# Kernel optimization log

Hardware: AMD Instinct MI355X
Metric: run time of the kernel (lower is better)

Reference implementation:

```python
import jax, jax.numpy as jnp
import numpy as np

D_MODEL = 512
NHEAD = 8
D_K = D_MODEL // NHEAD


def setup_inputs() -> dict:
    key = jax.random.key(0)
    ks = jax.random.split(key, 9)
    s = 1.0 / np.sqrt(D_MODEL)
    x = jax.random.normal(ks[0], (2, 2048, D_MODEL), dtype=jnp.float32)
    # torch Linear weights: [out_features, in_features]
    Wq = jax.random.uniform(ks[1], (D_MODEL, D_MODEL), jnp.float32, -s, s)
    bq = jax.random.uniform(ks[2], (D_MODEL,), jnp.float32, -s, s)
    Wk = jax.random.uniform(ks[3], (D_MODEL, D_MODEL), jnp.float32, -s, s)
    bk = jax.random.uniform(ks[4], (D_MODEL,), jnp.float32, -s, s)
    Wv = jax.random.uniform(ks[5], (D_MODEL, D_MODEL), jnp.float32, -s, s)
    bv = jax.random.uniform(ks[6], (D_MODEL,), jnp.float32, -s, s)
    Wo = jax.random.uniform(ks[7], (D_MODEL, D_MODEL), jnp.float32, -s, s)
    bo = jax.random.uniform(ks[8], (D_MODEL,), jnp.float32, -s, s)
    return {"x": x, "Wq": Wq, "bq": bq, "Wk": Wk, "bk": bk,
            "Wv": Wv, "bv": bv, "Wo": Wo, "bo": bo}


def reference(x, Wq, bq, Wk, bk, Wv, bv, Wo, bo):
    B, S, D = x.shape
    H, Dk = NHEAD, D_K

    def proj(W, b):
        # torch Linear: x @ W.T + b -> [B, S, D] -> [B, H, S, Dk]
        y = jnp.einsum('bsd,ed->bse', x, W) + b
        return y.reshape(B, S, H, Dk).transpose(0, 2, 1, 3)

    q = proj(Wq, bq)
    k = proj(Wk, bk)
    v = proj(Wv, bv)

    scores = jnp.einsum('bhqd,bhkd->bhqk', q, k) / jnp.sqrt(jnp.float32(Dk))
    attn = jax.nn.softmax(scores, axis=-1)  # explicit O(S^2) attention matrix
    out = jnp.einsum('bhqk,bhkd->bhqd', attn, v)
    out = out.transpose(0, 2, 1, 3).reshape(B, S, D)
    return jnp.einsum('bsd,ed->bse', out, Wo) + bo
```

## Files before the change

kernel.cpp:

```cpp
#include <hip/hip_runtime.h>

typedef __bf16 bf16_t;
typedef bf16_t bf16x8 __attribute__((ext_vector_type(8)));
typedef bf16_t bf16x4 __attribute__((ext_vector_type(4)));
typedef float  floatx4 __attribute__((ext_vector_type(4)));
typedef short  s16x4   __attribute__((ext_vector_type(4)));

#define D_MODEL 512
#define NHEAD   8
#define DK      64
#define BATCH   2
#define SEQ     2048
#define MTOT    (BATCH*SEQ)
#define QSCALE  0.18033688011112042591f

static __device__ __forceinline__ floatx4 mfma16(bf16x8 a, bf16x8 b, floatx4 c) {
    return __builtin_amdgcn_mfma_f32_16x16x32_bf16(a, b, c, 0, 0, 0);
}
static __device__ __forceinline__ floatx4 mfma16k16(s16x4 a, s16x4 b, floatx4 c) {
    return __builtin_amdgcn_mfma_f32_16x16x16bf16_1k(a, b, c, 0, 0, 0);
}

static __device__ __forceinline__ void glds16(bf16_t* lds, const bf16_t* g) {
    __builtin_amdgcn_global_load_lds(
        (const __attribute__((address_space(1))) unsigned int*)g,
        (__attribute__((address_space(3))) unsigned int*)lds,
        16, 0, 0);
}

__global__ __launch_bounds__(256)
void to_bf16(const float* __restrict__ x,
             const float* __restrict__ Wq, const float* __restrict__ Wk,
             const float* __restrict__ Wv, const float* __restrict__ Wo,
             bf16_t* __restrict__ xb, bf16_t* __restrict__ wqb,
             bf16_t* __restrict__ wkb, bf16_t* __restrict__ wvb,
             bf16_t* __restrict__ wob)
{
    const int blk = blockIdx.x;
    const float* src; bf16_t* dst; size_t base;
    if      (blk < 1024) { src = x;  dst = xb;  base = (size_t)blk * 2048; }
    else if (blk < 1152) { src = Wq; dst = wqb; base = (size_t)(blk - 1024) * 2048; }
    else if (blk < 1280) { src = Wk; dst = wkb; base = (size_t)(blk - 1152) * 2048; }
    else if (blk < 1408) { src = Wv; dst = wvb; base = (size_t)(blk - 1280) * 2048; }
    else                 { src = Wo; dst = wob; base = (size_t)(blk - 1408) * 2048; }
    const size_t off = base + (size_t)threadIdx.x * 8;
    const float4 a = *(const float4*)(src + off);
    const float4 b = *(const float4*)(src + off + 4);
    bf16x8 p;
    p[0]=(bf16_t)a.x; p[1]=(bf16_t)a.y; p[2]=(bf16_t)a.z; p[3]=(bf16_t)a.w;
    p[4]=(bf16_t)b.x; p[5]=(bf16_t)b.y; p[6]=(bf16_t)b.z; p[7]=(bf16_t)b.w;
    const size_t off2 = off ^ ((((off >> 10) & 3)) << 3);
    *(bf16x8*)(dst + off2) = p;
}

__global__ __launch_bounds__(256)
void qkv_proj(const bf16_t* __restrict__ xb,
              const bf16_t* __restrict__ wqb, const float* __restrict__ bq,
              const bf16_t* __restrict__ wkb, const float* __restrict__ bk,
              const bf16_t* __restrict__ wvb, const float* __restrict__ bv,
              bf16_t* __restrict__ q_ws, bf16_t* __restrict__ k_ws,
              bf16_t* __restrict__ vt_ws)
{
    __shared__ bf16_t As[64 * 32];
    __shared__ bf16_t Bs[128 * 32];

    const int mtile = blockIdx.x;
    const int ntile = blockIdx.y;
    const int which = ntile >> 2;
    const int nsub  = ntile & 3;
    const bf16_t* W   = (which == 0) ? wqb : (which == 1) ? wkb : wvb;
    const float* bias = (which == 0) ? bq  : (which == 1) ? bk  : bv;

    const int tid  = threadIdx.x;
    const int lane = tid & 63;
    const int wave = tid >> 6;
    const int wm = wave & 1, wn = wave >> 1;
    const int l15 = lane & 15, quad = lane >> 4;
    const int m0 = mtile * 64;
    const int n0 = nsub * 128;
    const int lr = lane >> 2;
    const int lc = (lane & 3) * 8;
    const int csw = (quad ^ ((l15 >> 1) & 3)) * 8;

    floatx4 acc[2][4] = {};

    for (int k0 = 0; k0 < 512; k0 += 32) {
        __syncthreads();
        glds16(&As[wave * 16 * 32], xb + (size_t)(m0 + wave * 16 + lr) * 512 + k0 + lc);
        #pragma unroll
        for (int q = 0; q < 2; ++q) {
            const int r = wave * 32 + q * 16;
            glds16(&Bs[r * 32], W + (size_t)(n0 + r + lr) * 512 + k0 + lc);
        }
        __syncthreads();

        bf16x8 af[2], bfr[4];
        #pragma unroll
        for (int i = 0; i < 2; ++i)
            af[i] = *(const bf16x8*)(&As[(wm * 32 + i * 16 + l15) * 32 + csw]);
        #pragma unroll
        for (int j = 0; j < 4; ++j)
            bfr[j] = *(const bf16x8*)(&Bs[(wn * 64 + j * 16 + l15) * 32 + csw]);
        #pragma unroll
        for (int i = 0; i < 2; ++i)
            #pragma unroll
            for (int j = 0; j < 4; ++j)
                acc[i][j] = mfma16(af[i], bfr[j], acc[i][j]);
    }

    #pragma unroll
    for (int j = 0; j < 4; ++j) {
        const int e = n0 + wn * 64 + j * 16 + l15;
        const float be = bias[e];
        const int h = e >> 6, d = e & 63;
        #pragma unroll
        for (int i = 0; i < 2; ++i) {
            const int mbase = m0 + wm * 32 + i * 16 + quad * 4;
            const int b = mbase >> 11;
            const int sl = mbase & 2047;
            floatx4 c = acc[i][j];
            if (which == 2) {
                bf16x4 pk;
                #pragma unroll
                for (int r = 0; r < 4; ++r) pk[r] = (bf16_t)(c[r] + be);
                const int slz = (sl & ~63) | ((((sl >> 3) & 7) ^ (d & 7)) << 3) | (sl & 7);
                *(bf16x4*)(vt_ws + ((size_t)((b * 8 + h) * 64 + d)) * 2048 + slz) = pk;
            } else if (which == 1) {
                #pragma unroll
                for (int r = 0; r < 4; ++r) {
                    const int s = sl + r;
                    const int dz = ((((d >> 3) ^ (s & 7))) << 3) | (d & 7);
                    k_ws[(size_t)(b * 8 + h) * (SEQ * DK) + (size_t)s * 64 + dz] =
                        (bf16_t)(c[r] + be);
                }
            } else {
                #pragma unroll
                for (int r = 0; r < 4; ++r)
                    q_ws[(size_t)(b * 8 + h) * (SEQ * DK) + (size_t)(sl + r) * 64 + d] =
                        (bf16_t)((c[r] + be) * QSCALE);
            }
        }
    }
}

__global__ __launch_bounds__(512, 4)
void attn_kernel(const bf16_t* __restrict__ q_ws, const bf16_t* __restrict__ k_ws,
                 const bf16_t* __restrict__ vt_ws, bf16_t* __restrict__ attn_ws)
{
    __shared__ bf16_t Kt[4][64 * 64];
    __shared__ bf16_t Vt[4][64 * 64];

    const int bh = blockIdx.x;
    const int qt = blockIdx.y;
    const int tid = threadIdx.x, lane = tid & 63, wave = tid >> 6;
    const int l15 = lane & 15, quad = lane >> 4;
    const int g  = wave & 3;
    const int wq = wave >> 2;

    const bf16_t* Qb  = q_ws  + (size_t)bh * SEQ * DK;
    const bf16_t* Kb  = k_ws  + (size_t)bh * SEQ * DK;
    const bf16_t* Vtb = vt_ws + (size_t)bh * DK * SEQ;

    const int sp = wave & 3;
    bf16_t* stile = (wave < 4) ? &Kt[sp][0] : &Vt[sp][0];
    const int srow8 = lane >> 3;
    const int scol  = (lane & 7) * 8;

    bf16x8 aq[2][2];
    #pragma unroll
    for (int mt = 0; mt < 2; ++mt)
        #pragma unroll
        for (int c = 0; c < 2; ++c)
            aq[mt][c] = *(const bf16x8*)(Qb +
                (size_t)(qt * 64 + wq * 32 + mt * 16 + l15) * 64 + c * 32 + quad * 8);

    floatx4 O[2][4] = {};
    float rs[2] = {0.f, 0.f};
    const int ksw0 = ((0 + quad) ^ (l15 & 7)) * 8;
    const int ksw1 = ((4 + quad) ^ (l15 & 7)) * 8;

    for (int t = 0; t < 8; ++t) {
        __syncthreads();
        {
            const int kg = t * 256 + sp * 64;
            if (wave < 4) {
                #pragma unroll
                for (int i = 0; i < 8; ++i)
                    glds16(stile + i * 512,
                           Kb + (size_t)(kg + i * 8 + srow8) * 64 + scol);
            } else {
                #pragma unroll
                for (int i = 0; i < 8; ++i)
                    glds16(stile + i * 512,
                           Vtb + (size_t)(i * 8 + srow8) * 2048 + kg + scol);
            }
        }
        __syncthreads();

        s16x4 pf[2][4];
        #pragma unroll
        for (int kf = 0; kf < 4; ++kf) {
            const bf16_t* krow = &Kt[g][(kf * 16 + l15) * 64];
            bf16x8 k0 = *(const bf16x8*)(krow + ksw0);
            bf16x8 k1 = *(const bf16x8*)(krow + ksw1);
            #pragma unroll
            for (int mt = 0; mt < 2; ++mt) {
                floatx4 z = {0.f, 0.f, 0.f, 0.f};
                z = mfma16(k0, aq[mt][0], z);
                z = mfma16(k1, aq[mt][1], z);
                bf16x4 pk;
                float s = 0.f;
                #pragma unroll
                for (int r = 0; r < 4; ++r) {
                    const float p = __builtin_amdgcn_exp2f(z[r]);
                    s += p;
                    pk[r] = (bf16_t)p;
                }
                rs[mt] += s;
                pf[mt][kf] = __builtin_bit_cast(s16x4, pk);
            }
        }

        #pragma unroll
        for (int kg2 = 0; kg2 < 4; ++kg2) {
            const int voff = (((kg2 * 2 + (quad >> 1)) ^ (l15 & 7)) * 8) + (quad & 1) * 4;
            #pragma unroll
            for (int df = 0; df < 4; ++df) {
                const s16x4 v = *(const s16x4*)(&Vt[g][(df * 16 + l15) * 64 + voff]);
                #pragma unroll
                for (int mt = 0; mt < 2; ++mt)
                    O[mt][df] = mfma16k16(pf[mt][kg2], v, O[mt][df]);
            }
        }
    }

    #pragma unroll
    for (int mt = 0; mt < 2; ++mt) {
        rs[mt] += __shfl_xor(rs[mt], 16, 64);
        rs[mt] += __shfl_xor(rs[mt], 32, 64);
    }

    float* scratch = (float*)&Kt[0][0];
    __syncthreads();
    if (g >= 2) {
        float* s = scratch + (size_t)((wq * 2 + (g - 2)) * 64 + lane) * 35;
        #pragma unroll
        for (int mt = 0; mt < 2; ++mt) {
            #pragma unroll
            for (int df = 0; df < 4; ++df)
                #pragma unroll
                for (int r = 0; r < 4; ++r) s[mt * 16 + df * 4 + r] = O[mt][df][r];
            s[32 + mt] = rs[mt];
        }
    }
    __syncthreads();
    if (g < 2) {
        const float* s = scratch + (size_t)((wq * 2 + g) * 64 + lane) * 35;
        #pragma unroll
        for (int mt = 0; mt < 2; ++mt) {
            #pragma unroll
            for (int df = 0; df < 4; ++df)
                #pragma unroll
                for (int r = 0; r < 4; ++r) O[mt][df][r] += s[mt * 16 + df * 4 + r];
            rs[mt] += s[32 + mt];
        }
    }
    __syncthreads();
    if (g == 1) {
        float* s = scratch + (size_t)(wq * 64 + lane) * 35;
        #pragma unroll
        for (int mt = 0; mt < 2; ++mt) {
            #pragma unroll
            for (int df = 0; df < 4; ++df)
                #pragma unroll
                for (int r = 0; r < 4; ++r) s[mt * 16 + df * 4 + r] = O[mt][df][r];
            s[32 + mt] = rs[mt];
        }
    }
    __syncthreads();
    if (g == 0) {
        const float* s = scratch + (size_t)(wq * 64 + lane) * 35;
        #pragma unroll
        for (int mt = 0; mt < 2; ++mt) {
            #pragma unroll
            for (int df = 0; df < 4; ++df)
                #pragma unroll
                for (int r = 0; r < 4; ++r) O[mt][df][r] += s[mt * 16 + df * 4 + r];
            rs[mt] += s[32 + mt];
        }

        const int b = bh >> 3, h = bh & 7;
        #pragma unroll
        for (int mt = 0; mt < 2; ++mt)
            #pragma unroll
            for (int r = 0; r < 4; ++r) {
                const float rv = __shfl(rs[mt], (quad << 4) + ((quad & 3) << 2) + r, 64);
                const float rinv = 1.0f / rv;
                const int s_ = qt * 64 + wq * 32 + mt * 16 + quad * 4 + r;
                const int sw = ((s_ >> 1) & 3) << 3;
                const size_t base = ((size_t)b * 2048 + s_) * 512;
                #pragma unroll
                for (int df = 0; df < 4; ++df) {
                    const int col = h * 64 + df * 16 + l15;
                    attn_ws[base + (col ^ sw)] = (bf16_t)(O[mt][df][r] * rinv);
                }
            }
    }
}

__global__ __launch_bounds__(256)
void out_proj(const bf16_t* __restrict__ attn_ws, const bf16_t* __restrict__ wob,
              const float* __restrict__ bo, float* __restrict__ y)
{
    __shared__ bf16_t As[64 * 32];
    __shared__ bf16_t Bs[128 * 32];

    const int mtile = blockIdx.x;
    const int ntile = blockIdx.y;
    const int tid = threadIdx.x, lane = tid & 63, wave = tid >> 6;
    const int wm = wave & 1, wn = wave >> 1;
    const int l15 = lane & 15, quad = lane >> 4;
    const int m0 = mtile * 64;
    const int n0 = ntile * 128;
    const int lr = lane >> 2, lc = (lane & 3) * 8;
    const int csw = (quad ^ ((l15 >> 1) & 3)) * 8;

    floatx4 acc[2][4] = {};

    for (int k0 = 0; k0 < 512; k0 += 32) {
        __syncthreads();
        glds16(&As[wave * 16 * 32], attn_ws + (size_t)(m0 + wave * 16 + lr) * 512 + k0 + lc);
        #pragma unroll
        for (int q = 0; q < 2; ++q) {
            const int r = wave * 32 + q * 16;
            glds16(&Bs[r * 32], wob + (size_t)(n0 + r + lr) * 512 + k0 + lc);
        }
        __syncthreads();

        bf16x8 af[2], bfr[4];
        #pragma unroll
        for (int i = 0; i < 2; ++i)
            af[i] = *(const bf16x8*)(&As[(wm * 32 + i * 16 + l15) * 32 + csw]);
        #pragma unroll
        for (int j = 0; j < 4; ++j)
            bfr[j] = *(const bf16x8*)(&Bs[(wn * 64 + j * 16 + l15) * 32 + csw]);
        #pragma unroll
        for (int i = 0; i < 2; ++i)
            #pragma unroll
            for (int j = 0; j < 4; ++j)
                acc[i][j] = mfma16(af[i], bfr[j], acc[i][j]);
    }

    #pragma unroll
    for (int j = 0; j < 4; ++j) {
        const int e = n0 + wn * 64 + j * 16 + l15;
        const float be = bo[e];
        #pragma unroll
        for (int i = 0; i < 2; ++i) {
            const int mb = m0 + wm * 32 + i * 16 + quad * 4;
            #pragma unroll
            for (int r = 0; r < 4; ++r)
                y[(size_t)(mb + r) * 512 + e] = acc[i][j][r] + be;
        }
    }
}

extern "C" void kernel_launch(void* const* d_in, const int* in_sizes, int n_in,
                              void* d_out, int out_size, void* d_ws, size_t ws_size,
                              hipStream_t stream) {
    (void)in_sizes; (void)n_in; (void)out_size; (void)ws_size;
    const float* x  = (const float*)d_in[0];
    const float* Wq = (const float*)d_in[1];
    const float* bq = (const float*)d_in[2];
    const float* Wk = (const float*)d_in[3];
    const float* bk = (const float*)d_in[4];
    const float* Wv = (const float*)d_in[5];
    const float* bv = (const float*)d_in[6];
    const float* Wo = (const float*)d_in[7];
    const float* bo = (const float*)d_in[8];

    bf16_t* xb   = (bf16_t*)d_ws;
    bf16_t* wqb  = xb   + (size_t)MTOT * D_MODEL;
    bf16_t* wkb  = wqb  + (size_t)D_MODEL * D_MODEL;
    bf16_t* wvb  = wkb  + (size_t)D_MODEL * D_MODEL;
    bf16_t* wob  = wvb  + (size_t)D_MODEL * D_MODEL;
    bf16_t* qws  = wob  + (size_t)D_MODEL * D_MODEL;
    bf16_t* kws  = qws  + (size_t)MTOT * D_MODEL;
    bf16_t* vtws = kws  + (size_t)MTOT * D_MODEL;
    bf16_t* aws  = vtws + (size_t)MTOT * D_MODEL;

    to_bf16    <<<1536, 256, 0, stream>>>(x, Wq, Wk, Wv, Wo, xb, wqb, wkb, wvb, wob);
    qkv_proj   <<<dim3(64, 12), 256, 0, stream>>>(xb, wqb, bq, wkb, bk, wvb, bv, qws, kws, vtws);
    attn_kernel<<<dim3(16, 32), 512, 0, stream>>>(qws, kws, vtws, aws);
    out_proj   <<<dim3(64, 4),  256, 0, stream>>>(aws, wob, bo, (float*)d_out);
}
```

Measured before the change: 130.1 us.

## Double-buffer LDS tiles in projections and attention, shrink attention blocks to 256 threads

The two projection GEMMs and the attention kernel now use ping-pong LDS buffers. The next K/V or weight tile is issued into the other buffer before the current one is computed on, so each iteration needs one barrier instead of two. The attention kernel drops from 8 to 4 waves per block, with 2 key groups instead of 4, 16 steps of 128 keys, and a simpler cross-wave reduction. The trade-offs are less per-block parallelism, different occupancy from the new launch bounds (256,2), and reliance on the barrier to make the async LDS loads visible.

```diff
diff --git a/kernel.cpp b/kernel.cpp
--- a/kernel.cpp
+++ b/kernel.cpp
@@ -61,8 +61,8 @@
               bf16_t* __restrict__ q_ws, bf16_t* __restrict__ k_ws,
               bf16_t* __restrict__ vt_ws)
 {
-    __shared__ bf16_t As[64 * 32];
-    __shared__ bf16_t Bs[128 * 32];
+    __shared__ bf16_t As[2][64 * 32];
+    __shared__ bf16_t Bs[2][128 * 32];
 
     const int mtile = blockIdx.x;
     const int ntile = blockIdx.y;
@@ -84,23 +84,36 @@
 
     floatx4 acc[2][4] = {};
 
-    for (int k0 = 0; k0 < 512; k0 += 32) {
-        __syncthreads();
-        glds16(&As[wave * 16 * 32], xb + (size_t)(m0 + wave * 16 + lr) * 512 + k0 + lc);
+    {
+        glds16(&As[0][wave * 16 * 32], xb + (size_t)(m0 + wave * 16 + lr) * 512 + lc);
         #pragma unroll
         for (int q = 0; q < 2; ++q) {
             const int r = wave * 32 + q * 16;
-            glds16(&Bs[r * 32], W + (size_t)(n0 + r + lr) * 512 + k0 + lc);
-        }
+            glds16(&Bs[0][r * 32], W + (size_t)(n0 + r + lr) * 512 + lc);
+        }
+    }
+
+    for (int kk = 0; kk < 16; ++kk) {
+        const int buf = kk & 1;
         __syncthreads();
+        if (kk < 15) {
+            const int kn = (kk + 1) * 32;
+            glds16(&As[buf ^ 1][wave * 16 * 32],
+                   xb + (size_t)(m0 + wave * 16 + lr) * 512 + kn + lc);
+            #pragma unroll
+            for (int q = 0; q < 2; ++q) {
+                const int r = wave * 32 + q * 16;
+                glds16(&Bs[buf ^ 1][r * 32], W + (size_t)(n0 + r + lr) * 512 + kn + lc);
+            }
+        }
 
         bf16x8 af[2], bfr[4];
         #pragma unroll
         for (int i = 0; i < 2; ++i)
-            af[i] = *(const bf16x8*)(&As[(wm * 32 + i * 16 + l15) * 32 + csw]);
+            af[i] = *(const bf16x8*)(&As[buf][(wm * 32 + i * 16 + l15) * 32 + csw]);
         #pragma unroll
         for (int j = 0; j < 4; ++j)
-            bfr[j] = *(const bf16x8*)(&Bs[(wn * 64 + j * 16 + l15) * 32 + csw]);
+            bfr[j] = *(const bf16x8*)(&Bs[buf][(wn * 64 + j * 16 + l15) * 32 + csw]);
         #pragma unroll
         for (int i = 0; i < 2; ++i)
             #pragma unroll
@@ -143,26 +156,26 @@
     }
 }
 
-__global__ __launch_bounds__(512, 4)
+__global__ __launch_bounds__(256, 2)
 void attn_kernel(const bf16_t* __restrict__ q_ws, const bf16_t* __restrict__ k_ws,
                  const bf16_t* __restrict__ vt_ws, bf16_t* __restrict__ attn_ws)
 {
-    __shared__ bf16_t Kt[4][64 * 64];
-    __shared__ bf16_t Vt[4][64 * 64];
+    __shared__ bf16_t Kt[2][2][64 * 64];
+    __shared__ bf16_t Vt[2][2][64 * 64];
 
     const int bh = blockIdx.x;
     const int qt = blockIdx.y;
     const int tid = threadIdx.x, lane = tid & 63, wave = tid >> 6;
     const int l15 = lane & 15, quad = lane >> 4;
-    const int g  = wave & 3;
-    const int wq = wave >> 2;
+    const int g  = wave >> 1;
+    const int wq = wave & 1;
 
     const bf16_t* Qb  = q_ws  + (size_t)bh * SEQ * DK;
     const bf16_t* Kb  = k_ws  + (size_t)bh * SEQ * DK;
     const bf16_t* Vtb = vt_ws + (size_t)bh * DK * SEQ;
 
-    const int sp = wave & 3;
-    bf16_t* stile = (wave < 4) ? &Kt[sp][0] : &Vt[sp][0];
+    const int sp = wave & 1;
+    const bool isK = wave < 2;
     const int srow8 = lane >> 3;
     const int scol  = (lane & 7) * 8;
 
@@ -179,28 +192,41 @@
     const int ksw0 = ((0 + quad) ^ (l15 & 7)) * 8;
     const int ksw1 = ((4 + quad) ^ (l15 & 7)) * 8;
 
-    for (int t = 0; t < 8; ++t) {
+    {
+        const int kg = sp * 64;
+        bf16_t* stile = isK ? &Kt[0][sp][0] : &Vt[0][sp][0];
+        if (isK) {
+            #pragma unroll
+            for (int i = 0; i < 8; ++i)
+                glds16(stile + i * 512, Kb + (size_t)(kg + i * 8 + srow8) * 64 + scol);
+        } else {
+            #pragma unroll
+            for (int i = 0; i < 8; ++i)
+                glds16(stile + i * 512, Vtb + (size_t)(i * 8 + srow8) * 2048 + kg + scol);
+        }
+    }
+
+    for (int t = 0; t < 16; ++t) {
+        const int buf = t & 1;
         __syncthreads();
-        {
-            const int kg = t * 256 + sp * 64;
-            if (wave < 4) {
+        if (t < 15) {
+            const int kg = (t + 1) * 128 + sp * 64;
+            bf16_t* stile = isK ? &Kt[buf ^ 1][sp][0] : &Vt[buf ^ 1][sp][0];
+            if (isK) {
                 #pragma unroll
                 for (int i = 0; i < 8; ++i)
-                    glds16(stile + i * 512,
-                           Kb + (size_t)(kg + i * 8 + srow8) * 64 + scol);
+                    glds16(stile + i * 512, Kb + (size_t)(kg + i * 8 + srow8) * 64 + scol);
             } else {
                 #pragma unroll
                 for (int i = 0; i < 8; ++i)
-                    glds16(stile + i * 512,
-                           Vtb + (size_t)(i * 8 + srow8) * 2048 + kg + scol);
-            }
-        }
-        __syncthreads();
+                    glds16(stile + i * 512, Vtb + (size_t)(i * 8 + srow8) * 2048 + kg + scol);
+            }
+        }
 
         s16x4 pf[2][4];
         #pragma unroll
         for (int kf = 0; kf < 4; ++kf) {
-            const bf16_t* krow = &Kt[g][(kf * 16 + l15) * 64];
+            const bf16_t* krow = &Kt[buf][g][(kf * 16 + l15) * 64];
             bf16x8 k0 = *(const bf16x8*)(krow + ksw0);
             bf16x8 k1 = *(const bf16x8*)(krow + ksw1);
             #pragma unroll
@@ -226,7 +252,7 @@
             const int voff = (((kg2 * 2 + (quad >> 1)) ^ (l15 & 7)) * 8) + (quad & 1) * 4;
             #pragma unroll
             for (int df = 0; df < 4; ++df) {
-                const s16x4 v = *(const s16x4*)(&Vt[g][(df * 16 + l15) * 64 + voff]);
+                const s16x4 v = *(const s16x4*)(&Vt[buf][g][(df * 16 + l15) * 64 + voff]);
                 #pragma unroll
                 for (int mt = 0; mt < 2; ++mt)
                     O[mt][df] = mfma16k16(pf[mt][kg2], v, O[mt][df]);
@@ -240,31 +266,7 @@
         rs[mt] += __shfl_xor(rs[mt], 32, 64);
     }
 
-    float* scratch = (float*)&Kt[0][0];
-    __syncthreads();
-    if (g >= 2) {
-        float* s = scratch + (size_t)((wq * 2 + (g - 2)) * 64 + lane) * 35;
-        #pragma unroll
-        for (int mt = 0; mt < 2; ++mt) {
-            #pragma unroll
-            for (int df = 0; df < 4; ++df)
-                #pragma unroll
-                for (int r = 0; r < 4; ++r) s[mt * 16 + df * 4 + r] = O[mt][df][r];
-            s[32 + mt] = rs[mt];
-        }
-    }
-    __syncthreads();
-    if (g < 2) {
-        const float* s = scratch + (size_t)((wq * 2 + g) * 64 + lane) * 35;
-        #pragma unroll
-        for (int mt = 0; mt < 2; ++mt) {
-            #pragma unroll
-            for (int df = 0; df < 4; ++df)
-                #pragma unroll
-                for (int r = 0; r < 4; ++r) O[mt][df][r] += s[mt * 16 + df * 4 + r];
-            rs[mt] += s[32 + mt];
-        }
-    }
+    float* scratch = (float*)&Kt[0][0][0];
     __syncthreads();
     if (g == 1) {
         float* s = scratch + (size_t)(wq * 64 + lane) * 35;
@@ -312,8 +314,8 @@
 void out_proj(const bf16_t* __restrict__ attn_ws, const bf16_t* __restrict__ wob,
               const float* __restrict__ bo, float* __restrict__ y)
 {
-    __shared__ bf16_t As[64 * 32];
-    __shared__ bf16_t Bs[128 * 32];
+    __shared__ bf16_t As[2][64 * 32];
+    __shared__ bf16_t Bs[2][128 * 32];
 
     const int mtile = blockIdx.x;
     const int ntile = blockIdx.y;
@@ -327,23 +329,36 @@
 
     floatx4 acc[2][4] = {};
 
-    for (int k0 = 0; k0 < 512; k0 += 32) {
-        __syncthreads();
-        glds16(&As[wave * 16 * 32], attn_ws + (size_t)(m0 + wave * 16 + lr) * 512 + k0 + lc);
+    {
+        glds16(&As[0][wave * 16 * 32], attn_ws + (size_t)(m0 + wave * 16 + lr) * 512 + lc);
         #pragma unroll
         for (int q = 0; q < 2; ++q) {
             const int r = wave * 32 + q * 16;
-            glds16(&Bs[r * 32], wob + (size_t)(n0 + r + lr) * 512 + k0 + lc);
-        }
+            glds16(&Bs[0][r * 32], wob + (size_t)(n0 + r + lr) * 512 + lc);
+        }
+    }
+
+    for (int kk = 0; kk < 16; ++kk) {
+        const int buf = kk & 1;
         __syncthreads();
+        if (kk < 15) {
+            const int kn = (kk + 1) * 32;
+            glds16(&As[buf ^ 1][wave * 16 * 32],
+                   attn_ws + (size_t)(m0 + wave * 16 + lr) * 512 + kn + lc);
+            #pragma unroll
+            for (int q = 0; q < 2; ++q) {
+                const int r = wave * 32 + q * 16;
+                glds16(&Bs[buf ^ 1][r * 32], wob + (size_t)(n0 + r + lr) * 512 + kn + lc);
+            }
+        }
 
         bf16x8 af[2], bfr[4];
         #pragma unroll
         for (int i = 0; i < 2; ++i)
-            af[i] = *(const bf16x8*)(&As[(wm * 32 + i * 16 + l15) * 32 + csw]);
+            af[i] = *(const bf16x8*)(&As[buf][(wm * 32 + i * 16 + l15) * 32 + csw]);
         #pragma unroll
         for (int j = 0; j < 4; ++j)
-            bfr[j] = *(const bf16x8*)(&Bs[(wn * 64 + j * 16 + l15) * 32 + csw]);
+            bfr[j] = *(const bf16x8*)(&Bs[buf][(wn * 64 + j * 16 + l15) * 32 + csw]);
         #pragma unroll
         for (int i = 0; i < 2; ++i)
             #pragma unroll
@@ -391,6 +406,6 @@
 
     to_bf16    <<<1536, 256, 0, stream>>>(x, Wq, Wk, Wv, Wo, xb, wqb, wkb, wvb, wob);
     qkv_proj   <<<dim3(64, 12), 256, 0, stream>>>(xb, wqb, bq, wkb, bk, wvb, bv, qws, kws, vtws);
-    attn_kernel<<<dim3(16, 32), 512, 0, stream>>>(qws, kws, vtws, aws);
+    attn_kernel<<<dim3(16, 32), 256, 0, stream>>>(qws, kws, vtws, aws);
     out_proj   <<<dim3(64, 4),  256, 0, stream>>>(aws, wob, bo, (float*)d_out);
 }
```

Measured after the change: 129.4 us. No clear change (-0.5%).
